# Performance work log

Measured on AMD Instinct MI355X. Metric: run time of the kernel, lower is better.

## Reference

```python
import jax, jax.numpy as jnp
import numpy as np

K = 10          # tagset_size (hardcoded default in CRF)
START_TAG = 8
STOP_TAG = 9
NEG = -10000.0  # value used by the torch code for impossible transitions


def setup_inputs() -> dict:
    key = jax.random.key(0)
    k1, k2, k3 = jax.random.split(key, 3)
    B, T = 4096, 700
    feats = jax.random.normal(k1, (B, T, K), dtype=jnp.float32)
    lengths = jax.random.randint(k2, (B,), 1, T + 1, dtype=jnp.int32)
    transitions = jax.random.normal(k3, (K, K), dtype=jnp.float32)
    # CRF.__init__: transitions[START_TAG, :] = -10000; transitions[:, STOP_TAG] = -10000
    transitions = transitions.at[START_TAG, :].set(NEG).at[:, STOP_TAG].set(NEG)
    return {"feats": feats, "lengths": lengths, "transitions": transitions}


def reference(feats, lengths, transitions):
    """CNN_CRF.forward (post-CNN): sequence-mask the features, then batched
    Viterbi decode (CRF._viterbi_decode_sequential) as a single lax.scan.
    Returns (path_scores [B], best_paths [B, T] int32, zero-padded past length)."""
    B, T, Kt = feats.shape
    mask = jnp.arange(T)[None, :] < lengths[:, None]          # [B, T]
    feats = feats * mask[..., None].astype(feats.dtype)       # cnn_features masking

    fv0 = jnp.full((B, Kt), NEG, dtype=feats.dtype).at[:, START_TAG].set(0.0)
    tag_ids = jnp.arange(Kt, dtype=jnp.int32)

    def step(fv, xs):
        feat_t, m_t = xs                                      # [B,K], [B]
        # next_tag_var[b, next, prev] = forward_var[b, prev] + transitions[next, prev]
        ntv = fv[:, None, :] + transitions[None, :, :]
        best = jnp.argmax(ntv, axis=2).astype(jnp.int32)      # [B, K] best prev per next
        vv = jnp.max(ntv, axis=2)                             # [B, K]
        fv_new = vv + feat_t                                  # emit added after max
        fv = jnp.where(m_t[:, None], fv_new, fv)              # freeze past length
        bp = jnp.where(m_t[:, None], best, tag_ids[None, :])  # identity bp past length
        return fv, bp

    fv, bps = jax.lax.scan(step, fv0, (jnp.swapaxes(feats, 0, 1), mask.T))  # bps: [T,B,K]

    terminal = fv + transitions[STOP_TAG][None, :]            # [B, K]
    path_scores = jnp.max(terminal, axis=1)                   # [B]
    last_tag = jnp.argmax(terminal, axis=1).astype(jnp.int32) # [B]

    b_idx = jnp.arange(B)

    def backtrace(tag, bp_t):
        out = tag                                             # tag at position t
        tag = bp_t[b_idx, tag]                                # tag at position t-1
        return tag, out

    _, path = jax.lax.scan(backtrace, last_tag, bps, reverse=True)  # [T, B]
    path = jnp.swapaxes(path, 0, 1)                           # [B, T]
    path = jnp.where(mask, path, 0)                           # zero padding past length
    return path_scores, path
```

## Files before the change

kernel.cpp:

```cpp
#include <hip/hip_runtime.h>
#include <stdint.h>

#define TAGS 10
#define START_TAG 8
#define STOP_TAG 9
#define NEGV (-10000.0f)

#define DPP_I(x, ctrl) __builtin_amdgcn_update_dpp(0, (x), (ctrl), 0xF, 0xF, true)

typedef int v4i __attribute__((ext_vector_type(4)));

__device__ __forceinline__ float maxf3(float a, float b, float c) {
    return fmaxf(fmaxf(a, b), c);
}

#define GLOADI(dst, base, OFF) \
    asm volatile("global_load_dword %0, %1, off offset:" #OFF \
                 : "=v"(dst) : "v"(base))
#define GLOADQ(dst, addr) \
    asm volatile("global_load_dwordx4 %0, %1, off" \
                 : "=v"(dst) : "v"((const void*)(addr)) : "memory")
#define GLOAD8(BUF, BASE) { \
    const float* gb_ = (BASE); \
    GLOADI(BUF[0], gb_, 0);   GLOADI(BUF[1], gb_, 40); \
    GLOADI(BUF[2], gb_, 80);  GLOADI(BUF[3], gb_, 120); \
    GLOADI(BUF[4], gb_, 160); GLOADI(BUF[5], gb_, 200); \
    GLOADI(BUF[6], gb_, 240); GLOADI(BUF[7], gb_, 280); }
#define GLOAD8X(BUF, FB, TB) { \
    GLOADI(BUF[0], (FB) + (size_t)min(max((TB) + 0, 0), T - 1) * TAGS, 0); \
    GLOADI(BUF[1], (FB) + (size_t)min(max((TB) + 1, 0), T - 1) * TAGS, 0); \
    GLOADI(BUF[2], (FB) + (size_t)min(max((TB) + 2, 0), T - 1) * TAGS, 0); \
    GLOADI(BUF[3], (FB) + (size_t)min(max((TB) + 3, 0), T - 1) * TAGS, 0); \
    GLOADI(BUF[4], (FB) + (size_t)min(max((TB) + 4, 0), T - 1) * TAGS, 0); \
    GLOADI(BUF[5], (FB) + (size_t)min(max((TB) + 5, 0), T - 1) * TAGS, 0); \
    GLOADI(BUF[6], (FB) + (size_t)min(max((TB) + 6, 0), T - 1) * TAGS, 0); \
    GLOADI(BUF[7], (FB) + (size_t)min(max((TB) + 7, 0), T - 1) * TAGS, 0); }
#define WAITP { asm volatile("s_waitcnt vmcnt(17)" ::: "memory"); \
                __builtin_amdgcn_sched_barrier(0); }
#define PINFENCE __builtin_amdgcn_sched_barrier(0);

__global__ __launch_bounds__(1024) void crf_sort(
    const int* __restrict__ lengths, int* __restrict__ ord, int B)
{
    __shared__ int hist[1024];
    __shared__ int offs[1024];
    const int tid = threadIdx.x;
    hist[tid] = 0;
    __syncthreads();
    for (int i = tid; i < B; i += 1024)
        atomicAdd(&hist[min(max(lengths[i], 0), 1023)], 1);
    __syncthreads();
    offs[tid] = hist[tid];
    __syncthreads();
    for (int off = 1; off < 1024; off <<= 1) {
        int v = (tid >= off) ? offs[tid - off] : 0;
        __syncthreads();
        offs[tid] += v;
        __syncthreads();
    }
    hist[tid] = offs[tid] - hist[tid];
    __syncthreads();
    for (int i = tid; i < B; i += 1024) {
        const int p = atomicAdd(&hist[min(max(lengths[i], 0), 1023)], 1);
        ord[p] = i;
    }
}

__global__ __launch_bounds__(64, 1) void crf_fb_fwd(
    const float* __restrict__ feats,
    const int*   __restrict__ lengths,
    const float* __restrict__ trans,
    const int*   __restrict__ ord,
    uint8_t*     __restrict__ bpA,
    uint8_t*     __restrict__ bpC,
    float*       __restrict__ fvAo,
    float*       __restrict__ hws,
    int B, int T, int H, int ABLK, int NCpad)
{
    const int lane = threadIdx.x & 63;
    const int grp  = lane >> 4;
    const int n    = lane & 15;
    const int m    = n & 7;
    const bool odd = (n & 1);

    int srcv[8];
    srcv[0] = n;
    srcv[1] = DPP_I(n, 0x121);  srcv[2] = DPP_I(n, 0x122);
    srcv[3] = DPP_I(n, 0x123);  srcv[4] = DPP_I(n, 0x124);
    srcv[5] = DPP_I(n, 0x125);  srcv[6] = DPP_I(n, 0x126);
    srcv[7] = DPP_I(n, 0x127);

    int rsrc[8];
#pragma unroll
    for (int r = 0; r < 8; ++r) rsrc[r] = (srcv[r] & 7) ^ 7;

    if ((int)blockIdx.x < ABLK) {
        const int b4   = blockIdx.x * 4;
        const int b    = ord[b4 + grp];
        const int len  = lengths[b];
        const int lenA = min(len, H);
        const int l0 = lengths[ord[b4 + 0]];
        const int l1 = lengths[ord[b4 + 1]];
        const int l2 = lengths[ord[b4 + 2]];
        const int l3 = lengths[ord[b4 + 3]];
        const int HA = min(max(max(l0, l1), max(l2, l3)), H);
        const int blocksA = H >> 3;

        float trowR[8];
#pragma unroll
        for (int r = 0; r < 8; ++r)
            trowR[r] = trans[m * TAGS + (srcv[r] & 7)];

        const float* fb = feats + (size_t)b * T * TAGS + m;
        uint8_t* bpa_l = bpA + (size_t)b * blocksA * 32 + ((n >> 1) & 3) * 8;
        const bool stl = (n < 8) && !odd;

        float fv = trans[m * TAGS + START_TAG] + fb[0];

#define KLEAF_A(r, ctrl) { \
        int rot_ = DPP_I(__float_as_int(fv), (ctrl)); \
        float lv_ = __int_as_float(rot_) + trowR[r]; \
        k##r = __int_as_float((__float_as_int(lv_) & ~7) | rsrc[r]); }

#define STEP_A(TI, FEAT, ACCST) { \
        const int t_ = (TI); \
        float k0, k1, k2, k3, k4, k5, k6, k7; \
        { float lv_ = fv + trowR[0]; \
          k0 = __int_as_float((__float_as_int(lv_) & ~7) | rsrc[0]); } \
        KLEAF_A(1, 0x121) KLEAF_A(2, 0x122) KLEAF_A(3, 0x123) \
        KLEAF_A(4, 0x124) KLEAF_A(5, 0x125) KLEAF_A(6, 0x126) \
        KLEAF_A(7, 0x127) \
        const float p1_ = maxf3(k0, k1, k2); \
        const float p2_ = maxf3(k3, k4, k5); \
        const float p3_ = maxf3(k6, k7, p1_); \
        const float mm_ = fmaxf(p2_, p3_); \
        const int idx_  = (__float_as_int(mm_) & 7) ^ 7; \
        const int pidx_ = DPP_I(idx_, 0xB1); \
        const uint32_t byte_ = (uint32_t)(odd ? (pidx_ | (idx_ << 4)) \
                                              : (idx_ | (pidx_ << 4))); \
        ACCST; \
        const float fvn_ = mm_ + (FEAT); \
        fv = ((unsigned)(t_ - 1) < (unsigned)(lenA - 1)) ? fvn_ : fv; }

#define PH_A(USE, LD, T0) { \
        GLOAD8(LD, fb + (size_t)min((T0) + 16, T - 8) * TAGS); \
        WAITP \
        uint32_t accl, acch; \
        STEP_A((T0) + 0, USE[0], accl = byte_) \
        STEP_A((T0) + 1, USE[1], accl |= byte_ << 8) \
        STEP_A((T0) + 2, USE[2], accl |= byte_ << 16) \
        STEP_A((T0) + 3, USE[3], accl |= byte_ << 24) \
        STEP_A((T0) + 4, USE[4], acch = byte_) \
        STEP_A((T0) + 5, USE[5], acch |= byte_ << 8) \
        STEP_A((T0) + 6, USE[6], acch |= byte_ << 16) \
        STEP_A((T0) + 7, USE[7], acch |= byte_ << 24) \
        if ((T0) < H) { \
            if (stl) *(uint2*)(bpa_l + (size_t)((T0) >> 3) * 32) \
                         = make_uint2(accl, acch); } }

        PINFENCE
        float xb[8], yb[8], zb[8];
        GLOAD8(xb, fb);
        GLOAD8(yb, fb + (size_t)min(8, T - 8) * TAGS);
        if (n < 8) *(volatile float*)(fvAo + (size_t)b * 8 + m) = 0.0f;

        for (int t0 = 0; t0 < HA; t0 += 24) {
            PH_A(xb, zb, t0)
            PH_A(yb, xb, t0 + 8)
            PH_A(zb, yb, t0 + 16)
        }
#undef KLEAF_A
#undef STEP_A
#undef PH_A

        if (n < 8)
            fvAo[(size_t)b * 8 + m] = fv;
    } else {
        const int g    = blockIdx.x - ABLK;
        const int c4   = (ABLK - 1 - g) * 4;
        const int b    = ord[c4 + grp];
        const int len  = lengths[b];
        const int lenm1 = len - 1;
        const int l0 = lengths[ord[c4 + 0]];
        const int l1 = lengths[ord[c4 + 1]];
        const int l2 = lengths[ord[c4 + 2]];
        const int l3 = lengths[ord[c4 + 3]];
        const int maxlen = max(max(l0, l1), max(l2, l3));

        const int ktop = (maxlen > H) ? min(NCpad - 1, (maxlen - H - 1) >> 3) : -1;
        const int k0 = ((ktop + 3) / 3) * 3 - 1;

        float trowC[8];
#pragma unroll
        for (int r = 0; r < 8; ++r)
            trowC[r] = trans[(srcv[r] & 7) * TAGS + m];

        float h = trans[STOP_TAG * TAGS + m];
        const float* fb = feats + (size_t)b * T * TAGS + m;
        uint8_t* bpc_l = bpC + (size_t)b * NCpad * 32 + ((n >> 1) & 3) * 8;
        const bool stl = (n < 8) && !odd;

#define KLEAF_C(r, ctrl) { \
        int rot_ = DPP_I(__float_as_int(e_), (ctrl)); \
        float lv_ = __int_as_float(rot_) + trowC[r]; \
        k##r = __int_as_float((__float_as_int(lv_) & ~7) | rsrc[r]); }

#define STEP_C(K, J, FEAT, ACCST) { \
        const int t_ = H - 1 + 8 * (K) + (J); \
        const float e_ = h + (FEAT); \
        float k0, k1, k2, k3, k4, k5, k6, k7; \
        { float lv_ = e_ + trowC[0]; \
          k0 = __int_as_float((__float_as_int(lv_) & ~7) | rsrc[0]); } \
        KLEAF_C(1, 0x121) KLEAF_C(2, 0x122) KLEAF_C(3, 0x123) \
        KLEAF_C(4, 0x124) KLEAF_C(5, 0x125) KLEAF_C(6, 0x126) \
        KLEAF_C(7, 0x127) \
        const float p1_ = maxf3(k0, k1, k2); \
        const float p2_ = maxf3(k3, k4, k5); \
        const float p3_ = maxf3(k6, k7, p1_); \
        const float mm_ = fmaxf(p2_, p3_); \
        const int idx_  = (__float_as_int(mm_) & 7) ^ 7; \
        const int pidx_ = DPP_I(idx_, 0xB1); \
        const uint32_t byte_ = (uint32_t)(odd ? (pidx_ | (idx_ << 4)) \
                                              : (idx_ | (pidx_ << 4))); \
        ACCST; \
        h = (t_ < lenm1) ? mm_ : h; }

#define PH_C(USE, LD, K) { \
        GLOAD8X(LD, fb, H + 8 * ((K) - 2)) \
        WAITP \
        uint32_t accl, acch; \
        STEP_C(K, 7, USE[7], acch = byte_ << 24) \
        STEP_C(K, 6, USE[6], acch |= byte_ << 16) \
        STEP_C(K, 5, USE[5], acch |= byte_ << 8) \
        STEP_C(K, 4, USE[4], acch |= byte_) \
        STEP_C(K, 3, USE[3], accl = byte_ << 24) \
        STEP_C(K, 2, USE[2], accl |= byte_ << 16) \
        STEP_C(K, 1, USE[1], accl |= byte_ << 8) \
        STEP_C(K, 0, USE[0], accl |= byte_) \
        if (stl) *(uint2*)(bpc_l + (size_t)(K) * 32) = make_uint2(accl, acch); }

        PINFENCE
        float xb[8], yb[8], zb[8];
        GLOAD8X(xb, fb, H + 8 * k0)
        GLOAD8X(yb, fb, H + 8 * (k0 - 1))
        if (n < 8) *(volatile float*)(hws + (size_t)b * 8 + m) = 0.0f;

        for (int k = k0; k >= 0; k -= 3) {
            PH_C(xb, zb, k)
            PH_C(yb, xb, k - 1)
            PH_C(zb, yb, k - 2)
        }
#undef KLEAF_C
#undef STEP_C
#undef PH_C

        if (n < 8)
            hws[(size_t)b * 8 + m] = h;
    }
}

#define CH_(QA, QB, J) { \
    const uint32_t sA_ = (tag & 2) ? (uint32_t)QA[2 + ((J) >> 2)] \
                                   : (uint32_t)QA[(J) >> 2]; \
    const uint32_t sB_ = (tag & 2) ? (uint32_t)QB[2 + ((J) >> 2)] \
                                   : (uint32_t)QB[(J) >> 2]; \
    const uint32_t sel_ = (tag & 4) ? sB_ : sA_; \
    chv_ = (int)((sel_ >> (8 * ((J) & 3) + 4 * (tag & 1))) & 7); }

#define AITER(K, QA, QB, VMC) { \
    asm volatile("s_waitcnt vmcnt(" #VMC ")" ::: "memory"); \
    __builtin_amdgcn_sched_barrier(0); \
    const int k_ = (K); \
    float bufv[8]; \
    _Pragma("unroll") \
    for (int u = 7; u >= 0; --u) { \
        const int t_ = 8 * k_ + u; \
        const bool act_ = t_ < lenA; \
        bufv[u] = act_ ? (float)tag : 0.0f; \
        int chv_; CH_(QA, QB, u) \
        tag = (act_ && t_ >= 1) ? chv_ : tag; \
    } \
    float4* o4_ = (float4*)(orow + 8 * k_); \
    o4_[0] = make_float4(bufv[0], bufv[1], bufv[2], bufv[3]); \
    o4_[1] = make_float4(bufv[4], bufv[5], bufv[6], bufv[7]); \
    const int kn_ = (k_ - 4 < 0) ? 0 : (k_ - 4); \
    GLOADQ(QA, ab8 + (size_t)kn_ * 32); \
    GLOADQ(QB, ab8 + (size_t)kn_ * 32 + 16); }

#define CITER(K, QA, QB, VMC) { \
    asm volatile("s_waitcnt vmcnt(" #VMC ")" ::: "memory"); \
    __builtin_amdgcn_sched_barrier(0); \
    const int k_ = (K); \
    float bufv[8]; \
    _Pragma("unroll") \
    for (int j = 0; j < 8; ++j) { \
        const int t_ = H - 1 + 8 * k_ + j; \
        const bool act_ = t_ < len - 1; \
        int chv_; CH_(QA, QB, j) \
        tag = act_ ? chv_ : tag; \
        bufv[j] = act_ ? (float)tag : 0.0f; \
    } \
    const int p0_ = H + 8 * k_; \
    if (p0_ + 7 < T) { \
        float4* o4_ = (float4*)(orow + p0_); \
        o4_[0] = make_float4(bufv[0], bufv[1], bufv[2], bufv[3]); \
        o4_[1] = make_float4(bufv[4], bufv[5], bufv[6], bufv[7]); \
    } else { \
        _Pragma("unroll") \
        for (int j = 0; j < 8; ++j) \
            if (p0_ + j < T) orow[p0_ + j] = bufv[j]; \
    } \
    const int kn_ = (k_ + 4 >= NCu) ? (NCu - 1) : (k_ + 4); \
    GLOADQ(QA, cb8 + (size_t)kn_ * 32); \
    GLOADQ(QB, cb8 + (size_t)kn_ * 32 + 16); }

__global__ __launch_bounds__(64, 1) void crf_fb_bt(
    const int*     __restrict__ lengths,
    const uint8_t* __restrict__ bpA,
    const uint8_t* __restrict__ bpC,
    const float*   __restrict__ fvA,
    const float*   __restrict__ hws,
    float*         __restrict__ out_scores,
    float*         __restrict__ out_path,
    int B, int T, int H, int NCpad)
{
    const int rb = (B + 63) >> 6;
    const bool roleA = ((int)blockIdx.x < rb);
    const int s = (roleA ? (int)blockIdx.x : (int)blockIdx.x - rb) * 64 + threadIdx.x;
    if (s >= B) return;
    const int len = lengths[s];
    const int blocksA = H >> 3;
    const int NCu = (T - H + 7) >> 3;

    float fa[8], hh[8];
    {
        const float4* f4 = (const float4*)(fvA + (size_t)s * 8);
        float4 a = f4[0], c = f4[1];
        fa[0]=a.x; fa[1]=a.y; fa[2]=a.z; fa[3]=a.w;
        fa[4]=c.x; fa[5]=c.y; fa[6]=c.z; fa[7]=c.w;
        const float4* h4 = (const float4*)(hws + (size_t)s * 8);
        float4 d = h4[0], e = h4[1];
        hh[0]=d.x; hh[1]=d.y; hh[2]=d.z; hh[3]=d.w;
        hh[4]=e.x; hh[5]=e.y; hh[6]=e.z; hh[7]=e.w;
    }
    float best = fa[0] + hh[0];
    int bstar = 0;
#pragma unroll
    for (int nn = 1; nn < 8; ++nn) {
        const float v = fa[nn] + hh[nn];
        if (v > best) { best = v; bstar = nn; }
    }

    float* orow = out_path + (size_t)s * T;
    int tag = bstar;
    v4i Q0a, Q0b, Q1a, Q1b, Q2a, Q2b, Q3a, Q3b;

    if (roleA) {
        const int lenA = min(len, H);
        const uint8_t* ab8 = bpA + (size_t)s * blocksA * 32;
        const int kt = blocksA - 1;
        GLOADQ(Q3a, ab8 + (size_t)kt * 32);       GLOADQ(Q3b, ab8 + (size_t)kt * 32 + 16);
        GLOADQ(Q2a, ab8 + (size_t)(kt - 1) * 32); GLOADQ(Q2b, ab8 + (size_t)(kt - 1) * 32 + 16);
        GLOADQ(Q1a, ab8 + (size_t)(kt - 2) * 32); GLOADQ(Q1b, ab8 + (size_t)(kt - 2) * 32 + 16);
        GLOADQ(Q0a, ab8 + (size_t)(kt - 3) * 32); GLOADQ(Q0b, ab8 + (size_t)(kt - 3) * 32 + 16);
        AITER(kt,     Q3a, Q3b, 6)
        AITER(kt - 1, Q2a, Q2b, 8)
        AITER(kt - 2, Q1a, Q1b, 10)
        AITER(kt - 3, Q0a, Q0b, 12)
        for (int k = kt - 4; k >= 3; k -= 4) {
            AITER(k,     Q3a, Q3b, 12)
            AITER(k - 1, Q2a, Q2b, 12)
            AITER(k - 2, Q1a, Q1b, 12)
            AITER(k - 3, Q0a, Q0b, 12)
        }
    } else {
        out_scores[s] = best;
        const uint8_t* cb8 = bpC + (size_t)s * NCpad * 32;
        GLOADQ(Q0a, cb8);                    GLOADQ(Q0b, cb8 + 16);
        GLOADQ(Q1a, cb8 + 32);               GLOADQ(Q1b, cb8 + 48);
        GLOADQ(Q2a, cb8 + 64);               GLOADQ(Q2b, cb8 + 80);
        GLOADQ(Q3a, cb8 + 96);               GLOADQ(Q3b, cb8 + 112);
        CITER(0, Q0a, Q0b, 6)
        CITER(1, Q1a, Q1b, 8)
        CITER(2, Q2a, Q2b, 10)
        CITER(3, Q3a, Q3b, 12)
        for (int k = 4; k + 3 < NCu; k += 4) {
            CITER(k,     Q0a, Q0b, 12)
            CITER(k + 1, Q1a, Q1b, 12)
            CITER(k + 2, Q2a, Q2b, 12)
            CITER(k + 3, Q3a, Q3b, 12)
        }
    }
}

__global__ __launch_bounds__(64, 1) void crf_fused_small(
    const float* __restrict__ feats,
    const int*   __restrict__ lengths,
    const float* __restrict__ trans,
    float*       __restrict__ out_scores,
    float*       __restrict__ out_path,
    uint8_t*     __restrict__ bp4,
    int B, int T)
{
    const int lane = threadIdx.x & 63;
    const int grp  = lane >> 4;
    const int n    = lane & 15;
    const int m    = n & 7;
    const bool odd = (n & 1);
    const int b4   = blockIdx.x * 4;
    const int b    = min(b4 + grp, B - 1);

    const int len = lengths[b];
    const int l0 = lengths[min(b4 + 0, B - 1)];
    const int l1 = lengths[min(b4 + 1, B - 1)];
    const int l2 = lengths[min(b4 + 2, B - 1)];
    const int l3 = lengths[min(b4 + 3, B - 1)];
    const int maxlen = max(max(l0, l1), max(l2, l3));

    int srcv[8];
    srcv[0] = n;
    srcv[1] = DPP_I(n, 0x121);  srcv[2] = DPP_I(n, 0x122);
    srcv[3] = DPP_I(n, 0x123);  srcv[4] = DPP_I(n, 0x124);
    srcv[5] = DPP_I(n, 0x125);  srcv[6] = DPP_I(n, 0x126);
    srcv[7] = DPP_I(n, 0x127);

    float trowR[8];
    int   rsrc[8];
#pragma unroll
    for (int r = 0; r < 8; ++r) {
        const int sq = srcv[r] & 7;
        trowR[r] = trans[m * TAGS + sq];
        rsrc[r]  = sq ^ 7;
    }

    const float* fb = feats + (size_t)b * T * TAGS + m;
    uint8_t* bpb = bp4 + (size_t)b * T * 4 + (n >> 1);
    const bool store_lane = (n < 8) && !odd;

    float fv = trans[m * TAGS + START_TAG] + fb[0];

#define KLEAF_S(r, ctrl) { \
        int rot_ = DPP_I(__float_as_int(fv), (ctrl)); \
        float lv_ = __int_as_float(rot_) + trowR[r]; \
        k##r = __int_as_float((__float_as_int(lv_) & ~7) | rsrc[r]); }

#define STEP_S(TI, FEAT) { \
        const int t_ = (TI); \
        float k0, k1, k2, k3, k4, k5, k6, k7; \
        { float lv_ = fv + trowR[0]; \
          k0 = __int_as_float((__float_as_int(lv_) & ~7) | rsrc[0]); } \
        KLEAF_S(1, 0x121) KLEAF_S(2, 0x122) KLEAF_S(3, 0x123) \
        KLEAF_S(4, 0x124) KLEAF_S(5, 0x125) KLEAF_S(6, 0x126) \
        KLEAF_S(7, 0x127) \
        const float p1_ = maxf3(k0, k1, k2); \
        const float p2_ = maxf3(k3, k4, k5); \
        const float p3_ = maxf3(k6, k7, p1_); \
        const float mm_ = fmaxf(p2_, p3_); \
        const int   idx_  = (__float_as_int(mm_) & 7) ^ 7; \
        const int   pidx_ = DPP_I(idx_, 0xB1); \
        const int   lo_   = odd ? pidx_ : idx_; \
        const int   hi_   = odd ? idx_ : pidx_; \
        const float fvn_  = mm_ + (FEAT); \
        fv = (t_ < len) ? fvn_ : fv; \
        if (t_ < T) { \
            if (store_lane) \
                bpb[(size_t)t_ * 4] = (uint8_t)(lo_ | (hi_ << 4)); \
        } }

    float fc[8], fn[8];
#pragma unroll
    for (int i = 0; i < 8; ++i)
        fc[i] = fb[(size_t)min(1 + i, T - 1) * TAGS];

    for (int t0 = 1; t0 < maxlen; t0 += 8) {
#pragma unroll
        for (int i = 0; i < 8; ++i)
            fn[i] = fb[(size_t)min(t0 + 8 + i, T - 1) * TAGS];

        STEP_S(t0 + 0, fc[0]) STEP_S(t0 + 1, fc[1])
        STEP_S(t0 + 2, fc[2]) STEP_S(t0 + 3, fc[3])
        STEP_S(t0 + 4, fc[4]) STEP_S(t0 + 5, fc[5])
        STEP_S(t0 + 6, fc[6]) STEP_S(t0 + 7, fc[7])

#pragma unroll
        for (int i = 0; i < 8; ++i) fc[i] = fn[i];
    }
#undef KLEAF_S
#undef STEP_S

    const float term = fv + trans[STOP_TAG * TAGS + m];
    float kk = __int_as_float((__float_as_int(term) & ~7) | (m ^ 7));
    kk = fmaxf(kk, __int_as_float(DPP_I(__float_as_int(kk), 0x124)));
    kk = fmaxf(kk, __int_as_float(DPP_I(__float_as_int(kk), 0x122)));
    kk = fmaxf(kk, __int_as_float(DPP_I(__float_as_int(kk), 0x121)));
    int tag = (__float_as_int(kk) & 7) ^ 7;

    if (n == 0)
        out_scores[b] = kk;

    __builtin_amdgcn_s_waitcnt(0);
    __builtin_amdgcn_sched_barrier(0);

    if (n == 0) {
        const uint32_t* rw = (const uint32_t*)(bp4 + (size_t)b * T * 4);
        float* orow = out_path + (size_t)b * T;
        const int NB = (T + 15) / 16;
        uint32_t wA[16], wB[16];

        auto loadblk = [&](int bi, uint32_t* w) {
            if (bi < 0) return;
#pragma unroll
            for (int j = 0; j < 4; ++j) {
                const int tb = min(bi * 16 + 4 * j, T - 4);
                *(uint4*)&w[4 * j] = *(const uint4*)&rw[tb];
            }
        };
        auto compblk = [&](int bi, uint32_t* w) {
            float buf[16];
#pragma unroll
            for (int u = 15; u >= 0; --u) {
                const int t = bi * 16 + u;
                if (t < T) {
                    const bool act = t < len;
                    buf[u] = act ? (float)tag : 0.0f;
                    if (act) tag = (int)((w[u] >> (4 * tag)) & 15);
                }
            }
#pragma unroll
            for (int j = 0; j < 16; j += 4) {
                const int t = bi * 16 + j;
                if (t + 3 < T)
                    *(float4*)(orow + t) = make_float4(buf[j], buf[j+1], buf[j+2], buf[j+3]);
            }
        };

        int bi = NB - 1;
        loadblk(bi, wA);
        loadblk(bi - 1, wB);
        for (; bi >= 0; bi -= 2) {
            compblk(bi, wA);
            loadblk(bi - 2, wA);
            if (bi - 1 >= 0) compblk(bi - 1, wB);
            loadblk(bi - 3, wB);
        }
    }
}

extern "C" void kernel_launch(void* const* d_in, const int* in_sizes, int n_in,
                              void* d_out, int out_size, void* d_ws, size_t ws_size,
                              hipStream_t stream)
{
    const float* feats   = (const float*)d_in[0];
    const int*   lengths = (const int*)d_in[1];
    const float* trans   = (const float*)d_in[2];
    const int B = in_sizes[1];
    const int T = in_sizes[0] / (B * TAGS);

    float* out_scores = (float*)d_out;
    float* out_path   = (float*)d_out + B;

    const int H = ((T / 2) + 15) & ~15;
    const int blocksA = H >> 3;
    const int NCu = (T - H + 7) >> 3;
    const int NCpad = ((NCu + 3) / 3) * 3;

    const size_t szA = (size_t)B * blocksA * 32;
    const size_t szC = (size_t)B * NCpad * 32;
    const size_t need = szA + szC + (size_t)B * 64 + (size_t)B * 4;

    const bool ok = (H >= 32) && (T > H + 1) && ((T & 3) == 0) && ((B & 3) == 0)
                    && ((blocksA & 3) == 0) && ((NCu & 3) == 0)
                    && (blocksA >= 8) && (NCu >= 8) && (need <= ws_size);

    if (ok) {
        uint8_t* bpA  = (uint8_t*)d_ws;
        uint8_t* bpC  = bpA + szA;
        float*   fvAo = (float*)(bpC + szC);
        float*   hws  = fvAo + (size_t)B * 8;
        int*     ord  = (int*)(hws + (size_t)B * 8);
        const int ABLK = B / 4;

        crf_sort<<<1, 1024, 0, stream>>>(lengths, ord, B);

        crf_fb_fwd<<<2 * ABLK, 64, 0, stream>>>(
            feats, lengths, trans, ord, bpA, bpC, fvAo, hws, B, T, H, ABLK, NCpad);

        const int rb = (B + 63) >> 6;
        crf_fb_bt<<<2 * rb, 64, 0, stream>>>(
            lengths, bpA, bpC, fvAo, hws, out_scores, out_path, B, T, H, NCpad);
    } else {
        uint8_t* bp4 = (uint8_t*)d_ws;
        crf_fused_small<<<(B + 3) / 4, 64, 0, stream>>>(
            feats, lengths, trans, out_scores, out_path, bp4, B, T);
    }
}
```

Before: 68.40 us.

## Fuse DPP rotations into v_add_f32_dpp and coarsen the length-sort histogram

The separate DPP move plus add in each Viterbi max-leaf is replaced by inline-asm v_add_f32_dpp with row_ror, so each rotation and add becomes one instruction on the serial recurrence chain. The per-step index XOR and the odd-lane select are removed: raw inverted indices are packed into the backpointer byte and un-inverted in the backtrace instead. The length sort now uses 64 coarse buckets (length>>4) with a wave-shuffle scan in place of a 1024-bin block scan, so sorting is approximate within buckets. The inline asm depends on a hand-placed s_nop for DPP hazards, and the packed byte order for odd lanes changes, which the backtrace must match.

```diff
diff --git a/kernel.cpp b/kernel.cpp
--- a/kernel.cpp
+++ b/kernel.cpp
@@ -39,29 +39,44 @@
                 __builtin_amdgcn_sched_barrier(0); }
 #define PINFENCE __builtin_amdgcn_sched_barrier(0);
 
+#define DPP7(SRC, TROW) \
+    asm("s_nop 1\n" \
+        "\tv_add_f32_dpp %0, %7, %8  row_ror:1 row_mask:0xf bank_mask:0xf\n" \
+        "\tv_add_f32_dpp %1, %7, %9  row_ror:2 row_mask:0xf bank_mask:0xf\n" \
+        "\tv_add_f32_dpp %2, %7, %10 row_ror:3 row_mask:0xf bank_mask:0xf\n" \
+        "\tv_add_f32_dpp %3, %7, %11 row_ror:4 row_mask:0xf bank_mask:0xf\n" \
+        "\tv_add_f32_dpp %4, %7, %12 row_ror:5 row_mask:0xf bank_mask:0xf\n" \
+        "\tv_add_f32_dpp %5, %7, %13 row_ror:6 row_mask:0xf bank_mask:0xf\n" \
+        "\tv_add_f32_dpp %6, %7, %14 row_ror:7 row_mask:0xf bank_mask:0xf\n" \
+        : "=&v"(l1), "=&v"(l2), "=&v"(l3), "=&v"(l4), \
+          "=&v"(l5), "=&v"(l6), "=&v"(l7) \
+        : "v"(SRC), "v"(TROW[1]), "v"(TROW[2]), "v"(TROW[3]), \
+          "v"(TROW[4]), "v"(TROW[5]), "v"(TROW[6]), "v"(TROW[7]));
+
 __global__ __launch_bounds__(1024) void crf_sort(
     const int* __restrict__ lengths, int* __restrict__ ord, int B)
 {
-    __shared__ int hist[1024];
-    __shared__ int offs[1024];
+    __shared__ int hist[64];
+    __shared__ int base[64];
     const int tid = threadIdx.x;
-    hist[tid] = 0;
+    if (tid < 64) hist[tid] = 0;
     __syncthreads();
     for (int i = tid; i < B; i += 1024)
-        atomicAdd(&hist[min(max(lengths[i], 0), 1023)], 1);
+        atomicAdd(&hist[min(lengths[i] >> 4, 63)], 1);
     __syncthreads();
-    offs[tid] = hist[tid];
-    __syncthreads();
-    for (int off = 1; off < 1024; off <<= 1) {
-        int v = (tid >= off) ? offs[tid - off] : 0;
-        __syncthreads();
-        offs[tid] += v;
-        __syncthreads();
-    }
-    hist[tid] = offs[tid] - hist[tid];
+    if (tid < 64) {
+        const int v = hist[tid];
+        int s = v;
+#pragma unroll
+        for (int off = 1; off < 64; off <<= 1) {
+            const int u = __shfl_up(s, off);
+            if (tid >= off) s += u;
+        }
+        base[tid] = s - v;
+    }
     __syncthreads();
     for (int i = tid; i < B; i += 1024) {
-        const int p = atomicAdd(&hist[min(max(lengths[i], 0), 1023)], 1);
+        const int p = atomicAdd(&base[min(lengths[i] >> 4, 63)], 1);
         ord[p] = i;
     }
 }
@@ -81,7 +96,6 @@
     const int grp  = lane >> 4;
     const int n    = lane & 15;
     const int m    = n & 7;
-    const bool odd = (n & 1);
 
     int srcv[8];
     srcv[0] = n;
@@ -100,10 +114,10 @@
         const int len  = lengths[b];
         const int lenA = min(len, H);
         const int l0 = lengths[ord[b4 + 0]];
-        const int l1 = lengths[ord[b4 + 1]];
-        const int l2 = lengths[ord[b4 + 2]];
-        const int l3 = lengths[ord[b4 + 3]];
-        const int HA = min(max(max(l0, l1), max(l2, l3)), H);
+        const int l1_ = lengths[ord[b4 + 1]];
+        const int l2_ = lengths[ord[b4 + 2]];
+        const int l3_ = lengths[ord[b4 + 3]];
+        const int HA = min(max(max(l0, l1_), max(l2_, l3_)), H);
         const int blocksA = H >> 3;
 
         float trowR[8];
@@ -113,31 +127,31 @@
 
         const float* fb = feats + (size_t)b * T * TAGS + m;
         uint8_t* bpa_l = bpA + (size_t)b * blocksA * 32 + ((n >> 1) & 3) * 8;
-        const bool stl = (n < 8) && !odd;
+        const bool stl = (n < 8) && !(n & 1);
 
         float fv = trans[m * TAGS + START_TAG] + fb[0];
-
-#define KLEAF_A(r, ctrl) { \
-        int rot_ = DPP_I(__float_as_int(fv), (ctrl)); \
-        float lv_ = __int_as_float(rot_) + trowR[r]; \
-        k##r = __int_as_float((__float_as_int(lv_) & ~7) | rsrc[r]); }
 
 #define STEP_A(TI, FEAT, ACCST) { \
         const int t_ = (TI); \
-        float k0, k1, k2, k3, k4, k5, k6, k7; \
+        float l1, l2, l3, l4, l5, l6, l7; \
+        DPP7(fv, trowR) \
+        float k0; \
         { float lv_ = fv + trowR[0]; \
           k0 = __int_as_float((__float_as_int(lv_) & ~7) | rsrc[0]); } \
-        KLEAF_A(1, 0x121) KLEAF_A(2, 0x122) KLEAF_A(3, 0x123) \
-        KLEAF_A(4, 0x124) KLEAF_A(5, 0x125) KLEAF_A(6, 0x126) \
-        KLEAF_A(7, 0x127) \
+        const float k1 = __int_as_float((__float_as_int(l1) & ~7) | rsrc[1]); \
+        const float k2 = __int_as_float((__float_as_int(l2) & ~7) | rsrc[2]); \
+        const float k3 = __int_as_float((__float_as_int(l3) & ~7) | rsrc[3]); \
+        const float k4 = __int_as_float((__float_as_int(l4) & ~7) | rsrc[4]); \
+        const float k5 = __int_as_float((__float_as_int(l5) & ~7) | rsrc[5]); \
+        const float k6 = __int_as_float((__float_as_int(l6) & ~7) | rsrc[6]); \
+        const float k7 = __int_as_float((__float_as_int(l7) & ~7) | rsrc[7]); \
         const float p1_ = maxf3(k0, k1, k2); \
         const float p2_ = maxf3(k3, k4, k5); \
         const float p3_ = maxf3(k6, k7, p1_); \
         const float mm_ = fmaxf(p2_, p3_); \
-        const int idx_  = (__float_as_int(mm_) & 7) ^ 7; \
-        const int pidx_ = DPP_I(idx_, 0xB1); \
-        const uint32_t byte_ = (uint32_t)(odd ? (pidx_ | (idx_ << 4)) \
-                                              : (idx_ | (pidx_ << 4))); \
+        const int xidx_ = __float_as_int(mm_) & 7;         \
+        const int pidx_ = DPP_I(xidx_, 0xB1); \
+        const uint32_t byte_ = (uint32_t)(xidx_ | (pidx_ << 4)); \
         ACCST; \
         const float fvn_ = mm_ + (FEAT); \
         fv = ((unsigned)(t_ - 1) < (unsigned)(lenA - 1)) ? fvn_ : fv; }
@@ -169,7 +183,6 @@
             PH_A(yb, xb, t0 + 8)
             PH_A(zb, yb, t0 + 16)
         }
-#undef KLEAF_A
 #undef STEP_A
 #undef PH_A
 
@@ -182,13 +195,13 @@
         const int len  = lengths[b];
         const int lenm1 = len - 1;
         const int l0 = lengths[ord[c4 + 0]];
-        const int l1 = lengths[ord[c4 + 1]];
-        const int l2 = lengths[ord[c4 + 2]];
-        const int l3 = lengths[ord[c4 + 3]];
-        const int maxlen = max(max(l0, l1), max(l2, l3));
+        const int l1_ = lengths[ord[c4 + 1]];
+        const int l2_ = lengths[ord[c4 + 2]];
+        const int l3_ = lengths[ord[c4 + 3]];
+        const int maxlen = max(max(l0, l1_), max(l2_, l3_));
 
         const int ktop = (maxlen > H) ? min(NCpad - 1, (maxlen - H - 1) >> 3) : -1;
-        const int k0 = ((ktop + 3) / 3) * 3 - 1;
+        const int k0i = ((ktop + 3) / 3) * 3 - 1;
 
         float trowC[8];
 #pragma unroll
@@ -198,30 +211,30 @@
         float h = trans[STOP_TAG * TAGS + m];
         const float* fb = feats + (size_t)b * T * TAGS + m;
         uint8_t* bpc_l = bpC + (size_t)b * NCpad * 32 + ((n >> 1) & 3) * 8;
-        const bool stl = (n < 8) && !odd;
-
-#define KLEAF_C(r, ctrl) { \
-        int rot_ = DPP_I(__float_as_int(e_), (ctrl)); \
-        float lv_ = __int_as_float(rot_) + trowC[r]; \
-        k##r = __int_as_float((__float_as_int(lv_) & ~7) | rsrc[r]); }
+        const bool stl = (n < 8) && !(n & 1);
 
 #define STEP_C(K, J, FEAT, ACCST) { \
         const int t_ = H - 1 + 8 * (K) + (J); \
         const float e_ = h + (FEAT); \
-        float k0, k1, k2, k3, k4, k5, k6, k7; \
+        float l1, l2, l3, l4, l5, l6, l7; \
+        DPP7(e_, trowC) \
+        float k0; \
         { float lv_ = e_ + trowC[0]; \
           k0 = __int_as_float((__float_as_int(lv_) & ~7) | rsrc[0]); } \
-        KLEAF_C(1, 0x121) KLEAF_C(2, 0x122) KLEAF_C(3, 0x123) \
-        KLEAF_C(4, 0x124) KLEAF_C(5, 0x125) KLEAF_C(6, 0x126) \
-        KLEAF_C(7, 0x127) \
+        const float k1 = __int_as_float((__float_as_int(l1) & ~7) | rsrc[1]); \
+        const float k2 = __int_as_float((__float_as_int(l2) & ~7) | rsrc[2]); \
+        const float k3 = __int_as_float((__float_as_int(l3) & ~7) | rsrc[3]); \
+        const float k4 = __int_as_float((__float_as_int(l4) & ~7) | rsrc[4]); \
+        const float k5 = __int_as_float((__float_as_int(l5) & ~7) | rsrc[5]); \
+        const float k6 = __int_as_float((__float_as_int(l6) & ~7) | rsrc[6]); \
+        const float k7 = __int_as_float((__float_as_int(l7) & ~7) | rsrc[7]); \
         const float p1_ = maxf3(k0, k1, k2); \
         const float p2_ = maxf3(k3, k4, k5); \
         const float p3_ = maxf3(k6, k7, p1_); \
         const float mm_ = fmaxf(p2_, p3_); \
-        const int idx_  = (__float_as_int(mm_) & 7) ^ 7; \
-        const int pidx_ = DPP_I(idx_, 0xB1); \
-        const uint32_t byte_ = (uint32_t)(odd ? (pidx_ | (idx_ << 4)) \
-                                              : (idx_ | (pidx_ << 4))); \
+        const int xidx_ = __float_as_int(mm_) & 7;         \
+        const int pidx_ = DPP_I(xidx_, 0xB1); \
+        const uint32_t byte_ = (uint32_t)(xidx_ | (pidx_ << 4)); \
         ACCST; \
         h = (t_ < lenm1) ? mm_ : h; }
 
@@ -241,16 +254,15 @@
 
         PINFENCE
         float xb[8], yb[8], zb[8];
-        GLOAD8X(xb, fb, H + 8 * k0)
-        GLOAD8X(yb, fb, H + 8 * (k0 - 1))
+        GLOAD8X(xb, fb, H + 8 * k0i)
+        GLOAD8X(yb, fb, H + 8 * (k0i - 1))
         if (n < 8) *(volatile float*)(hws + (size_t)b * 8 + m) = 0.0f;
 
-        for (int k = k0; k >= 0; k -= 3) {
+        for (int k = k0i; k >= 0; k -= 3) {
             PH_C(xb, zb, k)
             PH_C(yb, xb, k - 1)
             PH_C(zb, yb, k - 2)
         }
-#undef KLEAF_C
 #undef STEP_C
 #undef PH_C
 
@@ -265,7 +277,7 @@
     const uint32_t sB_ = (tag & 2) ? (uint32_t)QB[2 + ((J) >> 2)] \
                                    : (uint32_t)QB[(J) >> 2]; \
     const uint32_t sel_ = (tag & 4) ? sB_ : sA_; \
-    chv_ = (int)((sel_ >> (8 * ((J) & 3) + 4 * (tag & 1))) & 7); }
+    chv_ = (int)(((sel_ >> (8 * ((J) & 3) + 4 * (tag & 1))) & 7) ^ 7); }
 
 #define AITER(K, QA, QB, VMC) { \
     asm volatile("s_waitcnt vmcnt(" #VMC ")" ::: "memory"); \
```

Result: no change. 67.15 us (-1.8%).
